# Kernel optimization log

Measured on AMD Instinct MI355X. Metric: run time of the kernel, lower is better.

Reference implementation:

```python
import jax, jax.numpy as jnp
import numpy as np

D = 1024          # feature_dim
ROT = D // 2      # rotary applied to first feature_dim//2 channels (RotaryEmbedding(dim//2))
B, S = 4, 8192


def _l2norm(x, eps=1e-6):
    # cos_sim feature map: x / ||x||_2 along feature dim
    return x * jax.lax.rsqrt(jnp.sum(x * x, axis=-1, keepdims=True) + eps)


def _rotary(x, rot_dim):
    # lucidrains rotary-embedding-torch: interleaved pairs, partial rotary on first rot_dim dims
    seq = x.shape[-2]
    half = rot_dim // 2
    inv_freq = 1.0 / (10000.0 ** (jnp.arange(0, rot_dim, 2, dtype=jnp.float32) / rot_dim))  # [rot/2]
    freqs = jnp.arange(seq, dtype=jnp.float32)[:, None] * inv_freq[None, :]                  # [s, rot/2]
    freqs = jnp.repeat(freqs, 2, axis=-1)                                                     # [s, rot]
    cos, sin = jnp.cos(freqs), jnp.sin(freqs)
    xr, xp = x[..., :rot_dim], x[..., rot_dim:]
    x2 = xr.reshape(*xr.shape[:-1], half, 2)
    rh = jnp.stack([-x2[..., 1], x2[..., 0]], axis=-1).reshape(xr.shape)  # rotate_half, interleaved
    return jnp.concatenate([xr * cos + rh * sin, xp], axis=-1)


def _layernorm(x, g, b, eps=1e-5):
    mu = jnp.mean(x, axis=-1, keepdims=True)
    var = jnp.mean(jnp.square(x - mu), axis=-1, keepdims=True)
    return (x - mu) * jax.lax.rsqrt(var + eps) * g + b


def setup_inputs() -> dict:
    key = jax.random.key(0)
    k1, k2, k3 = jax.random.split(key, 3)
    X = jax.random.normal(k1, (B, S, D), jnp.float32)
    W_in = jax.random.normal(k2, (3 * D, D), jnp.float32) / np.float32(np.sqrt(D))
    W_out = jax.random.normal(k3, (D, D), jnp.float32) / np.float32(np.sqrt(D))
    ln_g = jnp.ones((D,), jnp.float32)
    ln_b = jnp.zeros((D,), jnp.float32)
    return {"X": X, "W_in": W_in, "W_out": W_out, "ln_g": ln_g, "ln_b": ln_b}


def reference(X, W_in, W_out, ln_g, ln_b):
    Xn = _layernorm(X, ln_g, ln_b)
    QKV = jnp.einsum('bsd,ed->bse', Xn, W_in)        # in_proj, no bias
    Q, K, V = jnp.split(QKV, 3, axis=-1)
    Q = _rotary(Q, ROT)
    K = _rotary(K, ROT)
    A = jnp.sum(_l2norm(K) * V, axis=-2)             # [b, d] global feature-map reduction
    Y = A[:, None, :] * _l2norm(Q)                   # feature_map_attn = identity
    Y = jnp.einsum('bsd,ed->bse', Y, W_out)          # out_proj, no bias
    return Y + X                                     # residual
```

## Files before the change

### kernel.cpp

```cpp
#include <hip/hip_runtime.h>

#define D 1024
#define S_LEN 8192
#define BATCH 4
#define NROWS (BATCH * S_LEN)

typedef unsigned short u16;
typedef __attribute__((ext_vector_type(8))) short short8;
typedef __attribute__((ext_vector_type(8))) unsigned short u16x8;
typedef __attribute__((ext_vector_type(4))) unsigned short u16x4;
typedef __attribute__((ext_vector_type(4))) float f32x4;

__device__ __forceinline__ float bf2f(u16 u) {
  return __builtin_bit_cast(float, ((unsigned)u) << 16);
}
__device__ __forceinline__ u16 f2bf(float f) {
  unsigned u = __builtin_bit_cast(unsigned, f);
  u += 0x7FFFu + ((u >> 16) & 1u);
  return (u16)(u >> 16);
}

#define GLD16(gp, lp)                                                    \
  __builtin_amdgcn_global_load_lds(                                      \
      (__attribute__((address_space(1))) void*)(void*)(gp),              \
      (__attribute__((address_space(3))) void*)(void*)(lp), 16, 0, 0)

__global__ __launch_bounds__(256) void tobf16_kernel(
    const float* __restrict__ src, u16* __restrict__ dst, int n4) {
  int t = blockIdx.x * 256 + threadIdx.x;
  if (t < n4) {
    float4 v = *(const float4*)&src[(size_t)t * 4];
    u16x4 o;
    o[0] = f2bf(v.x); o[1] = f2bf(v.y); o[2] = f2bf(v.z); o[3] = f2bf(v.w);
    *(u16x4*)&dst[(size_t)t * 4] = o;
  }
}

__global__ __launch_bounds__(256) void rope_table_kernel(
    float* __restrict__ ct, float* __restrict__ st) {
  int t = blockIdx.x * 256 + threadIdx.x;
  int s = t >> 8, j = t & 255;
  float invf = exp2f((float)j * -0.0519051265f);
  float f = (float)s * invf;
  float sv, cv;
  sincosf(f, &sv, &cv);
  ct[t] = cv;
  st[t] = sv;
}

__global__ __launch_bounds__(256) void ln_kernel(
    const float* __restrict__ X, const float* __restrict__ g,
    const float* __restrict__ bb, u16* __restrict__ Xn) {
  const int wave = threadIdx.x >> 6, lane = threadIdx.x & 63;
  const int row = blockIdx.x * 4 + wave;
  const float* xr = X + (size_t)row * D;
  float4 v[4];
  float s = 0.f, sq = 0.f;
#pragma unroll
  for (int i = 0; i < 4; i++) {
    v[i] = *(const float4*)&xr[lane * 4 + i * 256];
    s += v[i].x + v[i].y + v[i].z + v[i].w;
    sq += v[i].x * v[i].x + v[i].y * v[i].y + v[i].z * v[i].z + v[i].w * v[i].w;
  }
#pragma unroll
  for (int off = 32; off > 0; off >>= 1) {
    s += __shfl_xor(s, off);
    sq += __shfl_xor(sq, off);
  }
  const float mu = s * (1.f / D);
  const float var = sq * (1.f / D) - mu * mu;
  const float rstd = rsqrtf(var + 1e-5f);
#pragma unroll
  for (int i = 0; i < 4; i++) {
    const int c = lane * 4 + i * 256;
    float4 gg = *(const float4*)&g[c];
    float4 bv = *(const float4*)&bb[c];
    u16x4 o;
    o[0] = f2bf((v[i].x - mu) * rstd * gg.x + bv.x);
    o[1] = f2bf((v[i].y - mu) * rstd * gg.y + bv.y);
    o[2] = f2bf((v[i].z - mu) * rstd * gg.z + bv.z);
    o[3] = f2bf((v[i].w - mu) * rstd * gg.w + bv.w);
    *(u16x4*)&Xn[(size_t)row * D + c] = o;
  }
}

template <int EPI>
__global__ __launch_bounds__(256) void gemm_bt(
    const u16* __restrict__ A, const u16* __restrict__ Bm,
    u16* __restrict__ Cbf, const float* __restrict__ Xres,
    float* __restrict__ Cf, int K, int ldc) {
  __shared__ u16 smem[2 * 128 * 64];
  u16* As = smem;
  u16* Bs = smem + 128 * 64;
  const int tid = threadIdx.x;
  const int wave = tid >> 6, lane = tid & 63;
  const int wm = wave >> 1, wn = wave & 1;
  const int l15 = lane & 15, quad = lane >> 4;
  const int m0 = blockIdx.y * 128;
  const int n0 = blockIdx.x * 128;
  const int sw = l15 & 7;

  f32x4 acc[4][4] = {};

  for (int k0 = 0; k0 < K; k0 += 64) {
    __syncthreads();
#pragma unroll
    for (int i = 0; i < 4; i++) {
      const int c = i * 256 + tid;
      const int row = c >> 3;
      const int g = (c & 7) ^ (row & 7);
      GLD16(&A[(size_t)(m0 + row) * K + k0 + g * 8], &As[c * 8]);
      GLD16(&Bm[(size_t)(n0 + row) * K + k0 + g * 8], &Bs[c * 8]);
    }
    __syncthreads();
#pragma unroll
    for (int ks = 0; ks < 2; ks++) {
      short8 af[4], bfr[4];
#pragma unroll
      for (int i = 0; i < 4; i++)
        af[i] = *(const short8*)
            &As[(wm * 64 + i * 16 + l15) * 64 + (((ks * 4 + quad) ^ sw) << 3)];
#pragma unroll
      for (int j = 0; j < 4; j++)
        bfr[j] = *(const short8*)
            &Bs[(wn * 64 + j * 16 + l15) * 64 + (((ks * 4 + quad) ^ sw) << 3)];
#pragma unroll
      for (int i = 0; i < 4; i++)
#pragma unroll
        for (int j = 0; j < 4; j++)
          acc[i][j] = __builtin_amdgcn_mfma_f32_16x16x32_bf16(
              af[i], bfr[j], acc[i][j], 0, 0, 0);
    }
  }

  if constexpr (EPI == 0) {
    __syncthreads();
    u16* my = smem + wave * 4096;
#pragma unroll
    for (int i = 0; i < 4; i++)
#pragma unroll
      for (int j = 0; j < 4; j++)
#pragma unroll
        for (int r = 0; r < 4; r++)
          my[(i * 16 + quad * 4 + r) * 64 + j * 16 + l15] = f2bf(acc[i][j][r]);
    __syncthreads();
#pragma unroll
    for (int t = 0; t < 8; t++) {
      const int flat = t * 512 + lane * 8;
      const int r64 = flat >> 6, c64 = flat & 63;
      *(u16x8*)&Cbf[(size_t)(m0 + wm * 64 + r64) * ldc + n0 + wn * 64 + c64] =
          *(const u16x8*)&my[flat];
    }
  } else {
#pragma unroll
    for (int i = 0; i < 4; i++) {
#pragma unroll
      for (int r = 0; r < 4; r++) {
        const int row = m0 + wm * 64 + i * 16 + quad * 4 + r;
#pragma unroll
        for (int j = 0; j < 4; j++) {
          const int col = n0 + wn * 64 + j * 16 + l15;
          Cf[(size_t)row * ldc + col] =
              acc[i][j][r] + Xres[(size_t)row * ldc + col];
        }
      }
    }
  }
}

__global__ __launch_bounds__(256) void areduce_kernel(
    const u16* __restrict__ QKV, const float* __restrict__ ct,
    const float* __restrict__ st, float* __restrict__ Aout) {
  const int wave = threadIdx.x >> 6, lane = threadIdx.x & 63;
  const int b = blockIdx.x >> 8;
  const int chunk = blockIdx.x & 255;
  const int c0 = lane << 4;
  float acc[16];
#pragma unroll
  for (int i = 0; i < 16; i++) acc[i] = 0.f;

  for (int t = 0; t < 8; t++) {
    const int s = chunk * 32 + wave * 8 + t;
    const size_t base = ((size_t)b * S_LEN + s) * (3 * D);
    u16x8 ka = *(const u16x8*)&QKV[base + D + c0];
    u16x8 kb = *(const u16x8*)&QKV[base + D + c0 + 8];
    float kx[16];
#pragma unroll
    for (int i = 0; i < 8; i++) { kx[i] = bf2f(ka[i]); kx[8 + i] = bf2f(kb[i]); }
    if (lane < 32) {
      const int jb = c0 >> 1;
      const float* cp = &ct[(size_t)s * 256 + jb];
      const float* sp = &st[(size_t)s * 256 + jb];
#pragma unroll
      for (int p = 0; p < 8; p++) {
        float cv = cp[p], sv = sp[p];
        float e = kx[2 * p], o = kx[2 * p + 1];
        kx[2 * p] = e * cv - o * sv;
        kx[2 * p + 1] = o * cv + e * sv;
      }
    }
    float sq = 0.f;
#pragma unroll
    for (int i = 0; i < 16; i++) sq += kx[i] * kx[i];
#pragma unroll
    for (int off = 32; off > 0; off >>= 1) sq += __shfl_xor(sq, off);
    const float rn = rsqrtf(sq + 1e-6f);
    u16x8 va = *(const u16x8*)&QKV[base + 2 * D + c0];
    u16x8 vb = *(const u16x8*)&QKV[base + 2 * D + c0 + 8];
#pragma unroll
    for (int i = 0; i < 8; i++) {
      acc[i] += kx[i] * rn * bf2f(va[i]);
      acc[8 + i] += kx[8 + i] * rn * bf2f(vb[i]);
    }
  }

  __shared__ float red[D];
  if (wave == 0) {
#pragma unroll
    for (int i = 0; i < 16; i++) red[c0 + i] = acc[i];
  }
  __syncthreads();
  for (int w = 1; w < 4; w++) {
    if (wave == w) {
#pragma unroll
      for (int i = 0; i < 16; i++) red[c0 + i] += acc[i];
    }
    __syncthreads();
  }
  const int tid = threadIdx.x;
#pragma unroll
  for (int i = 0; i < 4; i++)
    atomicAdd(&Aout[(b << 10) + tid * 4 + i], red[tid * 4 + i]);
}

__global__ __launch_bounds__(256) void y_kernel(
    const u16* __restrict__ QKV, const float* __restrict__ ct,
    const float* __restrict__ st, const float* __restrict__ Ain,
    u16* __restrict__ Y) {
  const int wave = threadIdx.x >> 6, lane = threadIdx.x & 63;
  const int row = blockIdx.x * 4 + wave;
  const int b = row >> 13, s = row & (S_LEN - 1);
  const int c0 = lane << 4;
  const size_t base = (size_t)row * (3 * D);
  u16x8 qa = *(const u16x8*)&QKV[base + c0];
  u16x8 qb = *(const u16x8*)&QKV[base + c0 + 8];
  float qx[16];
#pragma unroll
  for (int i = 0; i < 8; i++) { qx[i] = bf2f(qa[i]); qx[8 + i] = bf2f(qb[i]); }
  if (lane < 32) {
    const int jb = c0 >> 1;
    const float* cp = &ct[(size_t)s * 256 + jb];
    const float* sp = &st[(size_t)s * 256 + jb];
#pragma unroll
    for (int p = 0; p < 8; p++) {
      float cv = cp[p], sv = sp[p];
      float e = qx[2 * p], o = qx[2 * p + 1];
      qx[2 * p] = e * cv - o * sv;
      qx[2 * p + 1] = o * cv + e * sv;
    }
  }
  float sq = 0.f;
#pragma unroll
  for (int i = 0; i < 16; i++) sq += qx[i] * qx[i];
#pragma unroll
  for (int off = 32; off > 0; off >>= 1) sq += __shfl_xor(sq, off);
  const float rn = rsqrtf(sq + 1e-6f);
  u16x8 oa, ob;
#pragma unroll
  for (int i = 0; i < 8; i++) {
    oa[i] = f2bf(Ain[(b << 10) + c0 + i] * qx[i] * rn);
    ob[i] = f2bf(Ain[(b << 10) + c0 + 8 + i] * qx[8 + i] * rn);
  }
  *(u16x8*)&Y[(size_t)row * D + c0] = oa;
  *(u16x8*)&Y[(size_t)row * D + c0 + 8] = ob;
}

extern "C" void kernel_launch(void* const* d_in, const int* in_sizes, int n_in,
                              void* d_out, int out_size, void* d_ws, size_t ws_size,
                              hipStream_t stream) {
  const float* X = (const float*)d_in[0];
  const float* W_in = (const float*)d_in[1];
  const float* W_out = (const float*)d_in[2];
  const float* ln_g = (const float*)d_in[3];
  const float* ln_b = (const float*)d_in[4];
  float* out = (float*)d_out;

  char* ws = (char*)d_ws;
  size_t off = 0;
  auto alloc = [&](size_t bytes) -> void* {
    void* p = ws + off;
    off += (bytes + 255) & ~(size_t)255;
    return p;
  };
  u16* QKV = (u16*)alloc((size_t)NROWS * 3 * D * 2);
  u16* Xn = (u16*)alloc((size_t)NROWS * D * 2);
  u16* Yb = (u16*)alloc((size_t)NROWS * D * 2);
  u16* Winb = (u16*)alloc((size_t)3 * D * D * 2);
  u16* Woutb = (u16*)alloc((size_t)D * D * 2);
  float* ct = (float*)alloc((size_t)S_LEN * 256 * 4);
  float* st = (float*)alloc((size_t)S_LEN * 256 * 4);
  float* Aacc = (float*)alloc((size_t)BATCH * D * 4);

  hipMemsetAsync(Aacc, 0, (size_t)BATCH * D * 4, stream);
  tobf16_kernel<<<3 * D * D / 1024, 256, 0, stream>>>(W_in, Winb, 3 * D * D / 4);
  tobf16_kernel<<<D * D / 1024, 256, 0, stream>>>(W_out, Woutb, D * D / 4);
  rope_table_kernel<<<S_LEN, 256, 0, stream>>>(ct, st);
  ln_kernel<<<NROWS / 4, 256, 0, stream>>>(X, ln_g, ln_b, Xn);

  dim3 g1(3 * D / 128, NROWS / 128);
  gemm_bt<0><<<g1, 256, 0, stream>>>(Xn, Winb, QKV, nullptr, nullptr, D, 3 * D);

  areduce_kernel<<<BATCH * 256, 256, 0, stream>>>(QKV, ct, st, Aacc);
  y_kernel<<<NROWS / 4, 256, 0, stream>>>(QKV, ct, st, Aacc, Yb);

  dim3 g2(D / 128, NROWS / 128);
  gemm_bt<1><<<g2, 256, 0, stream>>>(Yb, Woutb, nullptr, X, out, D, D);
}
```

Baseline: 670.5 us.

## Fuse prep kernels into one launch and replace atomics with two-stage reduction

Merges layernorm, rope table generation and both weight bf16 conversions into a single prep kernel dispatched by block index, which removes several launches and the memset. Rope tables now use range-reduced sinpif/cospif in place of sincosf. The areduce kernel writes per-block partial sums to a workspace buffer after a single-sync shared reduction, and a small afinal kernel sums them deterministically, replacing global atomics and the serialized shared reduction. This costs extra workspace traffic and one more launch for the final reduce.

New measurement: 650.5 us. 3.0% less time.

```diff
diff --git a/kernel.cpp b/kernel.cpp
--- a/kernel.cpp
+++ b/kernel.cpp
@@ -25,62 +25,72 @@
       (__attribute__((address_space(1))) void*)(void*)(gp),              \
       (__attribute__((address_space(3))) void*)(void*)(lp), 16, 0, 0)
 
-__global__ __launch_bounds__(256) void tobf16_kernel(
-    const float* __restrict__ src, u16* __restrict__ dst, int n4) {
-  int t = blockIdx.x * 256 + threadIdx.x;
-  if (t < n4) {
-    float4 v = *(const float4*)&src[(size_t)t * 4];
+__global__ __launch_bounds__(256) void prep_kernel(
+    const float* __restrict__ X, const float* __restrict__ g,
+    const float* __restrict__ bb, u16* __restrict__ Xn,
+    float* __restrict__ ct, float* __restrict__ st,
+    const float* __restrict__ Wa, u16* __restrict__ da, int n4a,
+    const float* __restrict__ Wb, u16* __restrict__ db, int n4b) {
+  const int bid = blockIdx.x;
+  const int tid = threadIdx.x;
+  if (bid < 8192) {
+    const int wave = tid >> 6, lane = tid & 63;
+    const int row = bid * 4 + wave;
+    const float* xr = X + (size_t)row * D;
+    float4 v[4];
+    float s = 0.f, sq = 0.f;
+#pragma unroll
+    for (int i = 0; i < 4; i++) {
+      v[i] = *(const float4*)&xr[lane * 4 + i * 256];
+      s += v[i].x + v[i].y + v[i].z + v[i].w;
+      sq += v[i].x * v[i].x + v[i].y * v[i].y + v[i].z * v[i].z + v[i].w * v[i].w;
+    }
+#pragma unroll
+    for (int off = 32; off > 0; off >>= 1) {
+      s += __shfl_xor(s, off);
+      sq += __shfl_xor(sq, off);
+    }
+    const float mu = s * (1.f / D);
+    const float var = sq * (1.f / D) - mu * mu;
+    const float rstd = rsqrtf(var + 1e-5f);
+#pragma unroll
+    for (int i = 0; i < 4; i++) {
+      const int c = lane * 4 + i * 256;
+      float4 gg = *(const float4*)&g[c];
+      float4 bv = *(const float4*)&bb[c];
+      u16x4 o;
+      o[0] = f2bf((v[i].x - mu) * rstd * gg.x + bv.x);
+      o[1] = f2bf((v[i].y - mu) * rstd * gg.y + bv.y);
+      o[2] = f2bf((v[i].z - mu) * rstd * gg.z + bv.z);
+      o[3] = f2bf((v[i].w - mu) * rstd * gg.w + bv.w);
+      *(u16x4*)&Xn[(size_t)row * D + c] = o;
+    }
+  } else if (bid < 16384) {
+    const int t = (bid - 8192) * 256 + tid;
+    const int s = t >> 8, j = t & 255;
+    const float invf = exp2f((float)j * -0.0519051265f);
+    const float f = (float)s * invf;
+    float rev = f * 0.15915494309189535f;
+    rev -= floorf(rev);
+    ct[t] = cospif(2.f * rev);
+    st[t] = sinpif(2.f * rev);
+  } else {
+    int t = (bid - 16384) * 256 + tid;
+    const float* sp;
+    u16* d;
+    if (t < n4a) {
+      sp = Wa + (size_t)t * 4;
+      d = da + (size_t)t * 4;
+    } else {
+      t -= n4a;
+      if (t >= n4b) return;
+      sp = Wb + (size_t)t * 4;
+      d = db + (size_t)t * 4;
+    }
+    float4 v = *(const float4*)sp;
     u16x4 o;
     o[0] = f2bf(v.x); o[1] = f2bf(v.y); o[2] = f2bf(v.z); o[3] = f2bf(v.w);
-    *(u16x4*)&dst[(size_t)t * 4] = o;
-  }
-}
-
-__global__ __launch_bounds__(256) void rope_table_kernel(
-    float* __restrict__ ct, float* __restrict__ st) {
-  int t = blockIdx.x * 256 + threadIdx.x;
-  int s = t >> 8, j = t & 255;
-  float invf = exp2f((float)j * -0.0519051265f);
-  float f = (float)s * invf;
-  float sv, cv;
-  sincosf(f, &sv, &cv);
-  ct[t] = cv;
-  st[t] = sv;
-}
-
-__global__ __launch_bounds__(256) void ln_kernel(
-    const float* __restrict__ X, const float* __restrict__ g,
-    const float* __restrict__ bb, u16* __restrict__ Xn) {
-  const int wave = threadIdx.x >> 6, lane = threadIdx.x & 63;
-  const int row = blockIdx.x * 4 + wave;
-  const float* xr = X + (size_t)row * D;
-  float4 v[4];
-  float s = 0.f, sq = 0.f;
-#pragma unroll
-  for (int i = 0; i < 4; i++) {
-    v[i] = *(const float4*)&xr[lane * 4 + i * 256];
-    s += v[i].x + v[i].y + v[i].z + v[i].w;
-    sq += v[i].x * v[i].x + v[i].y * v[i].y + v[i].z * v[i].z + v[i].w * v[i].w;
-  }
-#pragma unroll
-  for (int off = 32; off > 0; off >>= 1) {
-    s += __shfl_xor(s, off);
-    sq += __shfl_xor(sq, off);
-  }
-  const float mu = s * (1.f / D);
-  const float var = sq * (1.f / D) - mu * mu;
-  const float rstd = rsqrtf(var + 1e-5f);
-#pragma unroll
-  for (int i = 0; i < 4; i++) {
-    const int c = lane * 4 + i * 256;
-    float4 gg = *(const float4*)&g[c];
-    float4 bv = *(const float4*)&bb[c];
-    u16x4 o;
-    o[0] = f2bf((v[i].x - mu) * rstd * gg.x + bv.x);
-    o[1] = f2bf((v[i].y - mu) * rstd * gg.y + bv.y);
-    o[2] = f2bf((v[i].z - mu) * rstd * gg.z + bv.z);
-    o[3] = f2bf((v[i].w - mu) * rstd * gg.w + bv.w);
-    *(u16x4*)&Xn[(size_t)row * D + c] = o;
+    *(u16x4*)d = o;
   }
 }
 
@@ -170,7 +180,7 @@
 
 __global__ __launch_bounds__(256) void areduce_kernel(
     const u16* __restrict__ QKV, const float* __restrict__ ct,
-    const float* __restrict__ st, float* __restrict__ Aout) {
+    const float* __restrict__ st, float* __restrict__ Apart) {
   const int wave = threadIdx.x >> 6, lane = threadIdx.x & 63;
   const int b = blockIdx.x >> 8;
   const int chunk = blockIdx.x & 255;
@@ -214,23 +224,34 @@
     }
   }
 
-  __shared__ float red[D];
-  if (wave == 0) {
-#pragma unroll
-    for (int i = 0; i < 16; i++) red[c0 + i] = acc[i];
-  }
+  __shared__ float red[4][D];
+#pragma unroll
+  for (int i = 0; i < 4; i++)
+    *(float4*)&red[wave][c0 + i * 4] =
+        make_float4(acc[i * 4], acc[i * 4 + 1], acc[i * 4 + 2], acc[i * 4 + 3]);
   __syncthreads();
-  for (int w = 1; w < 4; w++) {
-    if (wave == w) {
-#pragma unroll
-      for (int i = 0; i < 16; i++) red[c0 + i] += acc[i];
-    }
-    __syncthreads();
-  }
   const int tid = threadIdx.x;
-#pragma unroll
-  for (int i = 0; i < 4; i++)
-    atomicAdd(&Aout[(b << 10) + tid * 4 + i], red[tid * 4 + i]);
+  float4 s0 = *(const float4*)&red[0][tid * 4];
+  float4 s1 = *(const float4*)&red[1][tid * 4];
+  float4 s2 = *(const float4*)&red[2][tid * 4];
+  float4 s3 = *(const float4*)&red[3][tid * 4];
+  float4 o;
+  o.x = s0.x + s1.x + s2.x + s3.x;
+  o.y = s0.y + s1.y + s2.y + s3.y;
+  o.z = s0.z + s1.z + s2.z + s3.z;
+  o.w = s0.w + s1.w + s2.w + s3.w;
+  *(float4*)&Apart[((size_t)blockIdx.x << 10) + tid * 4] = o;
+}
+
+__global__ __launch_bounds__(256) void afinal_kernel(
+    const float* __restrict__ Apart, float* __restrict__ Aout) {
+  const int e = blockIdx.x * 256 + threadIdx.x;
+  const int b = e >> 10, d = e & 1023;
+  const float* p = Apart + ((size_t)b << 18) + d;
+  float s = 0.f;
+#pragma unroll 8
+  for (int c = 0; c < 256; c++) s += p[(size_t)c << 10];
+  Aout[e] = s;
 }
 
 __global__ __launch_bounds__(256) void y_kernel(
@@ -299,18 +320,18 @@
   u16* Woutb = (u16*)alloc((size_t)D * D * 2);
   float* ct = (float*)alloc((size_t)S_LEN * 256 * 4);
   float* st = (float*)alloc((size_t)S_LEN * 256 * 4);
+  float* Apart = (float*)alloc((size_t)BATCH * 256 * D * 4);
   float* Aacc = (float*)alloc((size_t)BATCH * D * 4);
 
-  hipMemsetAsync(Aacc, 0, (size_t)BATCH * D * 4, stream);
-  tobf16_kernel<<<3 * D * D / 1024, 256, 0, stream>>>(W_in, Winb, 3 * D * D / 4);
-  tobf16_kernel<<<D * D / 1024, 256, 0, stream>>>(W_out, Woutb, D * D / 4);
-  rope_table_kernel<<<S_LEN, 256, 0, stream>>>(ct, st);
-  ln_kernel<<<NROWS / 4, 256, 0, stream>>>(X, ln_g, ln_b, Xn);
+  const int n4a = 3 * D * D / 4, n4b = D * D / 4;
+  prep_kernel<<<20480, 256, 0, stream>>>(X, ln_g, ln_b, Xn, ct, st, W_in, Winb,
+                                         n4a, W_out, Woutb, n4b);
 
   dim3 g1(3 * D / 128, NROWS / 128);
   gemm_bt<0><<<g1, 256, 0, stream>>>(Xn, Winb, QKV, nullptr, nullptr, D, 3 * D);
 
-  areduce_kernel<<<BATCH * 256, 256, 0, stream>>>(QKV, ct, st, Aacc);
+  areduce_kernel<<<BATCH * 256, 256, 0, stream>>>(QKV, ct, st, Apart);
+  afinal_kernel<<<16, 256, 0, stream>>>(Apart, Aacc);
   y_kernel<<<NROWS / 4, 256, 0, stream>>>(QKV, ct, st, Aacc, Yb);
 
   dim3 g2(D / 128, NROWS / 128);
```
